# Kernel tuning notes

Hardware: AMD Instinct MI355X
Metric: run time of the kernel (lower is better)

## Reference

```python
import jax, jax.numpy as jnp
import numpy as np

SEQ, BATCH, INPUT, HIDDEN, OUTPUT = 4096, 512, 8, 30, 1


def setup_inputs() -> dict:
    key = jax.random.key(0)
    ks = jax.random.split(key, 8)
    s = 1.0 / np.sqrt(HIDDEN)  # torch LSTM/Linear init scale
    u = lambda k, shape: jax.random.uniform(k, shape, jnp.float32, -s, s)
    return {
        "x": jax.random.normal(ks[0], (SEQ, BATCH, INPUT), jnp.float32),
        "W_ih": u(ks[1], (4 * HIDDEN, INPUT)),   # gate order: i, f, g, o
        "W_hh": u(ks[2], (4 * HIDDEN, HIDDEN)),
        "b_ih": u(ks[3], (4 * HIDDEN,)),
        "b_hh": u(ks[4], (4 * HIDDEN,)),
        "W_lin": u(ks[5], (OUTPUT, HIDDEN)),
        "b_lin": u(ks[6], (OUTPUT,)),
    }


def _lstm(x, W_ih, W_hh, b_ih, b_hh):
    H = W_hh.shape[1]
    B = x.shape[1]
    # Precompute input projections for all timesteps: [S,B,4H]
    x_proj = jnp.einsum("sbi,gi->sbg", x, W_ih) + b_ih + b_hh

    def step(carry, xp_t):
        h, c = carry
        gates = xp_t + h @ W_hh.T  # [B,4H]
        i, f, g, o = jnp.split(gates, 4, axis=-1)
        i, f, o = jax.nn.sigmoid(i), jax.nn.sigmoid(f), jax.nn.sigmoid(o)
        c = f * c + i * jnp.tanh(g)
        h = o * jnp.tanh(c)
        return (h, c), h

    h0 = jnp.zeros((B, H), x.dtype)
    c0 = jnp.zeros((B, H), x.dtype)
    _, pred = jax.lax.scan(step, (h0, c0), x_proj)
    return pred  # [S,B,H]


def reference(x, W_ih, W_hh, b_ih, b_hh, W_lin, b_lin):
    pred = _lstm(x, W_ih, W_hh, b_ih, b_hh)
    # per-timestep Linear (loop in the original == one batched matmul)
    out = jnp.einsum("sbh,oh->sbo", pred, W_lin) + b_lin
    return out
```

## Files before the change

kernel.cpp:

```cpp
#include <hip/hip_runtime.h>

#define SEQ 4096
#define BATCH 512
#define INP 8
#define HID 30
#define LOG2E 1.44269504088896340736f

typedef float f32x2 __attribute__((ext_vector_type(2)));
typedef float f32x4 __attribute__((ext_vector_type(4)));
typedef unsigned uint2v __attribute__((ext_vector_type(2)));

#define RCP(v)  __builtin_amdgcn_rcpf(v)
#if __has_builtin(__builtin_amdgcn_exp2f)
#define EXP2(v) __builtin_amdgcn_exp2f(v)
#else
#define EXP2(v) exp2f(v)
#endif
#define PKFMA(a, b, c) __builtin_elementwise_fma(a, b, c)

__device__ __forceinline__ void rep_halves(float v, float& lo_rep, float& hi_rep) {
#if __has_builtin(__builtin_amdgcn_permlane32_swap)
    uint2v r = __builtin_amdgcn_permlane32_swap(
        __float_as_uint(v), __float_as_uint(v), false, false);
    lo_rep = __uint_as_float(r.x);
    hi_rep = __uint_as_float(r.y);
#else
    float other = __shfl_xor(v, 32, 64);
    bool hi = (threadIdx.x & 32) != 0;
    lo_rep = hi ? other : v;
    hi_rep = hi ? v : other;
#endif
}

template <int CTRL>
__device__ __forceinline__ float dpp_sum_step(float v) {
    return v + __uint_as_float(__builtin_amdgcn_update_dpp(
        0, (int)__float_as_uint(v), CTRL, 0xf, 0xf, true));
}

__device__ __forceinline__ float group32_reduce(float v) {
    v = dpp_sum_step<0x111>(v);
    v = dpp_sum_step<0x112>(v);
    v = dpp_sum_step<0x114>(v);
    v = dpp_sum_step<0x118>(v);
#if __has_builtin(__builtin_amdgcn_permlane16_swap)
    uint2v r = __builtin_amdgcn_permlane16_swap(
        __float_as_uint(v), __float_as_uint(v), false, false);
    return __uint_as_float(r.x) + __uint_as_float(r.y);
#else
    return v + __shfl_xor(v, 16, 64);
#endif
}

__global__ __launch_bounds__(64)
__attribute__((amdgpu_waves_per_eu(1, 1)))
void lstm_chain_kernel(
    const float* __restrict__ x,
    const float* __restrict__ W_ih,
    const float* __restrict__ W_hh,
    const float* __restrict__ b_ih,
    const float* __restrict__ b_hh,
    const float* __restrict__ W_lin,
    const float* __restrict__ b_lin,
    float* __restrict__ out)
{
    const int lane = threadIdx.x;
    const int g    = blockIdx.x;
    const int b    = (g & 7) * (BATCH / 8) + (g >> 3);
    const int j    = lane & 31;
    const int half = lane >> 5;
    const int jc   = j < HID ? j : HID - 1;
    const int ra   = half * HID + jc;
    const int rb   = 2 * HID + half * HID + jc;

    const float sA   = -LOG2E;
    const float sB   = half ? -LOG2E : 2.0f * LOG2E;
    const float sclB = half ? 1.0f : -2.0f;
    const float addB = half ? 0.0f : 1.0f;
    const float T2L  = 2.0f * LOG2E;

    f32x2 wih2_a[INP / 2], wih2_b[INP / 2];
#pragma unroll
    for (int i = 0; i < INP / 2; ++i) {
        f32x2 wa = { W_ih[ra * INP + 2 * i] * sA, W_ih[ra * INP + 2 * i + 1] * sA };
        f32x2 wb = { W_ih[rb * INP + 2 * i] * sB, W_ih[rb * INP + 2 * i + 1] * sB };
        asm volatile("" : "+v"(wa));
        asm volatile("" : "+v"(wb));
        wih2_a[i] = wa;
        wih2_b[i] = wb;
    }
    f32x2 whh2_a[HID / 2], whh2_b[HID / 2];
#pragma unroll
    for (int k = 0; k < HID / 2; ++k) {
        f32x2 wa = { W_hh[ra * HID + 2 * k] * sA, W_hh[ra * HID + 2 * k + 1] * sA };
        f32x2 wb = { W_hh[rb * HID + 2 * k] * sB, W_hh[rb * HID + 2 * k + 1] * sB };
        asm volatile("" : "+v"(wa));
        asm volatile("" : "+v"(wb));
        whh2_a[k] = wa;
        whh2_b[k] = wb;
    }
    const float bias_sa = (b_ih[ra] + b_hh[ra]) * sA;
    const float bias_sb = (b_ih[rb] + b_hh[rb]) * sB;
    const float blin    = b_lin[0];
    const float wlin    = (j < HID) ? W_lin[j] : 0.0f;

    __shared__ float s_y[SEQ];
    __shared__ __align__(16) float s_h[64];
    __shared__ __align__(16) float s_x[2 * 64 * INP];

    f32x4* sx4 = reinterpret_cast<f32x4*>(s_x);
    const f32x4* sx4c = reinterpret_cast<const f32x4*>(s_x);

    f32x2 hrf2[HID / 2];
#pragma unroll
    for (int k = 0; k < HID / 2; ++k) hrf2[k] = (f32x2){0.0f, 0.0f};
    float c = 0.0f;

    f32x4 stg0, stg1;

#define STAGELOAD(CH2) do {                                                   \
    int _b0 = (CH2) * 64 + (lane >> 1);                                       \
    int _b1 = _b0 + 32;                                                       \
    if (_b0 > SEQ - 1) _b0 = SEQ - 1;                                         \
    if (_b1 > SEQ - 1) _b1 = SEQ - 1;                                         \
    const f32x4* _p0 = (const f32x4*)(x + ((size_t)_b0 * BATCH + b) * INP) + (lane & 1); \
    const f32x4* _p1 = (const f32x4*)(x + ((size_t)_b1 * BATCH + b) * INP) + (lane & 1); \
    stg0 = *_p0;                                                              \
    stg1 = *_p1;                                                              \
} while (0)

#define STAGEWRITE(CHW) do {                                                  \
    f32x4* _d = sx4 + ((CHW) & 1) * 128;                                      \
    _d[lane]      = stg0;                                                     \
    _d[64 + lane] = stg1;                                                     \
} while (0)

#define LOADXL(XA, XB, TL) do {                                               \
    int _e = (((TL) >> 6) & 1) * 128 + ((TL) & 63) * 2;                       \
    XA = sx4c[_e];                                                            \
    XB = sx4c[_e + 1];                                                        \
} while (0)

    STAGELOAD(0);
    STAGEWRITE(0);
    STAGELOAD(1);

    f32x4 xA0, xB0, xA1, xB1, xA2, xB2, xA3, xB3;
    LOADXL(xA0, xB0, 0);  LOADXL(xA1, xB1, 1);
    LOADXL(xA2, xB2, 2);  LOADXL(xA3, xB3, 3);

    const f32x4* s_h4 = reinterpret_cast<const f32x4*>(s_h);

#define STEP(T, XA, XB) do {                                                  \
    f32x2 A0 = {bias_sa, 0.0f}, B0 = {bias_sb, 0.0f};                         \
    f32x2 A1 = {0.0f, 0.0f},    B1 = {0.0f, 0.0f};                            \
    f32x2 x01 = __builtin_shufflevector(XA, XA, 0, 1);                        \
    f32x2 x23 = __builtin_shufflevector(XA, XA, 2, 3);                        \
    f32x2 x45 = __builtin_shufflevector(XB, XB, 0, 1);                        \
    f32x2 x67 = __builtin_shufflevector(XB, XB, 2, 3);                        \
    A0 = PKFMA(x01, wih2_a[0], A0);  B0 = PKFMA(x01, wih2_b[0], B0);          \
    A1 = PKFMA(x23, wih2_a[1], A1);  B1 = PKFMA(x23, wih2_b[1], B1);          \
    A0 = PKFMA(x45, wih2_a[2], A0);  B0 = PKFMA(x45, wih2_b[2], B0);          \
    A1 = PKFMA(x67, wih2_a[3], A1);  B1 = PKFMA(x67, wih2_b[3], B1);          \
    _Pragma("unroll")                                                         \
    for (int k = 0; k < HID / 2 - 1; k += 2) {                                \
        A0 = PKFMA(hrf2[k],   whh2_a[k],   A0);                               \
        B0 = PKFMA(hrf2[k],   whh2_b[k],   B0);                               \
        A1 = PKFMA(hrf2[k+1], whh2_a[k+1], A1);                               \
        B1 = PKFMA(hrf2[k+1], whh2_b[k+1], B1);                               \
    }                                                                         \
    A0 = PKFMA(hrf2[HID/2-1], whh2_a[HID/2-1], A0);                           \
    B0 = PKFMA(hrf2[HID/2-1], whh2_b[HID/2-1], B0);                           \
    f32x2 As = A0 + A1;  float ua = As.x + As.y;                              \
    f32x2 Bs = B0 + B1;  float ub = Bs.x + Bs.y;                              \
    float Av  = RCP(1.0f + EXP2(ua));                                         \
    float sBv = RCP(1.0f + EXP2(ub));                                         \
    float Bv  = fmaf(sBv, sclB, addB);                                        \
    float ii, ff, gg, oo;                                                     \
    rep_halves(Av, ii, ff);                                                   \
    rep_halves(Bv, gg, oo);                                                   \
    c = fmaf(ff, c, ii * gg);                                                 \
    float sc = RCP(1.0f + EXP2(c * T2L));                                     \
    float h  = oo * fmaf(sc, -2.0f, 1.0f);                                    \
    s_h[lane] = h;             \
    asm volatile("" ::: "memory");         \
    float p = group32_reduce(h * wlin);                                       \
    if (lane == 31) s_y[T] = p + blin;                                        \
    f32x4 hv0 = s_h4[0], hv1 = s_h4[1], hv2 = s_h4[2], hv3 = s_h4[3];         \
    f32x4 hv4 = s_h4[4], hv5 = s_h4[5], hv6 = s_h4[6], hv7 = s_h4[7];         \
    hrf2[0]  = __builtin_shufflevector(hv0, hv0, 0, 1);                       \
    hrf2[1]  = __builtin_shufflevector(hv0, hv0, 2, 3);                       \
    hrf2[2]  = __builtin_shufflevector(hv1, hv1, 0, 1);                       \
    hrf2[3]  = __builtin_shufflevector(hv1, hv1, 2, 3);                       \
    hrf2[4]  = __builtin_shufflevector(hv2, hv2, 0, 1);                       \
    hrf2[5]  = __builtin_shufflevector(hv2, hv2, 2, 3);                       \
    hrf2[6]  = __builtin_shufflevector(hv3, hv3, 0, 1);                       \
    hrf2[7]  = __builtin_shufflevector(hv3, hv3, 2, 3);                       \
    hrf2[8]  = __builtin_shufflevector(hv4, hv4, 0, 1);                       \
    hrf2[9]  = __builtin_shufflevector(hv4, hv4, 2, 3);                       \
    hrf2[10] = __builtin_shufflevector(hv5, hv5, 0, 1);                       \
    hrf2[11] = __builtin_shufflevector(hv5, hv5, 2, 3);                       \
    hrf2[12] = __builtin_shufflevector(hv6, hv6, 0, 1);                       \
    hrf2[13] = __builtin_shufflevector(hv6, hv6, 2, 3);                       \
    hrf2[14] = __builtin_shufflevector(hv7, hv7, 0, 1);                       \
} while (0)

    for (int ch = 0; ch < SEQ / 64; ++ch) {
        STAGEWRITE(ch + 1);
        STAGELOAD(ch + 2);
        const int t0 = ch * 64;
#pragma unroll 1
        for (int tt = 0; tt < 64; tt += 4) {
            const int t = t0 + tt;
            STEP(t + 0, xA0, xB0);  LOADXL(xA0, xB0, t + 4);
            STEP(t + 1, xA1, xB1);  LOADXL(xA1, xB1, t + 5);
            STEP(t + 2, xA2, xB2);  LOADXL(xA2, xB2, t + 6);
            STEP(t + 3, xA3, xB3);  LOADXL(xA3, xB3, t + 7);
        }
    }
#undef STEP
#undef LOADXL
#undef STAGELOAD
#undef STAGEWRITE

    __syncthreads();
    const float4* s_y4 = reinterpret_cast<const float4*>(s_y);
#pragma unroll 4
    for (int it = 0; it < SEQ / 256; ++it) {
        int tbase = it * 256 + lane * 4;
        float4 v = s_y4[tbase >> 2];
        out[(size_t)(tbase + 0) * BATCH + b] = v.x;
        out[(size_t)(tbase + 1) * BATCH + b] = v.y;
        out[(size_t)(tbase + 2) * BATCH + b] = v.z;
        out[(size_t)(tbase + 3) * BATCH + b] = v.w;
    }
}

extern "C" void kernel_launch(void* const* d_in, const int* in_sizes, int n_in,
                              void* d_out, int out_size, void* d_ws, size_t ws_size,
                              hipStream_t stream) {
    const float* x     = (const float*)d_in[0];
    const float* W_ih  = (const float*)d_in[1];
    const float* W_hh  = (const float*)d_in[2];
    const float* b_ih  = (const float*)d_in[3];
    const float* b_hh  = (const float*)d_in[4];
    const float* W_lin = (const float*)d_in[5];
    const float* b_lin = (const float*)d_in[6];
    float* out = (float*)d_out;

    lstm_chain_kernel<<<dim3(BATCH), dim3(64), 0, stream>>>(
        x, W_ih, W_hh, b_ih, b_hh, W_lin, b_lin, out);
}
```

Measured before the change: 1.034 ms.

## Precompute next-step input projection off the critical path and fold tanh scaling

Moves the input-projection FMAs for step t+1 into step t, placed after the hidden-state LDS write so they overlap the LDS round trip and reduction latency. The cell state is carried pre-scaled by 2*log2e so the tanh exponent needs no multiply, and the output gate is folded into a single FMA for h. The compiler memory barrier after the s_h store is removed and the h reads are issued right after the write. This relies on LDS ordering within a single wave and adds a few registers for the precomputed accumulators.

Result: faster. 945.3 us (-8.6%).

```diff
diff --git a/kernel.cpp b/kernel.cpp
--- a/kernel.cpp
+++ b/kernel.cpp
@@ -75,9 +75,10 @@
 
     const float sA   = -LOG2E;
     const float sB   = half ? -LOG2E : 2.0f * LOG2E;
-    const float sclB = half ? 1.0f : -2.0f;
-    const float addB = half ? 0.0f : 1.0f;
     const float T2L  = 2.0f * LOG2E;
+    const float IT2L = 1.0f / (2.0f * LOG2E);
+    const float sclB2 = half ? T2L : -2.0f * T2L;
+    const float addB2 = half ? 0.0f : T2L;
 
     f32x2 wih2_a[INP / 2], wih2_b[INP / 2];
 #pragma unroll
@@ -114,7 +115,7 @@
     f32x2 hrf2[HID / 2];
 #pragma unroll
     for (int k = 0; k < HID / 2; ++k) hrf2[k] = (f32x2){0.0f, 0.0f};
-    float c = 0.0f;
+    float c2 = 0.0f;
 
     f32x4 stg0, stg1;
 
@@ -141,27 +142,34 @@
     XB = sx4c[_e + 1];                                                        \
 } while (0)
 
-    STAGELOAD(0);
-    STAGEWRITE(0);
-    STAGELOAD(1);
-
-    f32x4 xA0, xB0, xA1, xB1, xA2, xB2, xA3, xB3;
-    LOADXL(xA0, xB0, 0);  LOADXL(xA1, xB1, 1);
-    LOADXL(xA2, xB2, 2);  LOADXL(xA3, xB3, 3);
-
-    const f32x4* s_h4 = reinterpret_cast<const f32x4*>(s_h);
-
-#define STEP(T, XA, XB) do {                                                  \
-    f32x2 A0 = {bias_sa, 0.0f}, B0 = {bias_sb, 0.0f};                         \
-    f32x2 A1 = {0.0f, 0.0f},    B1 = {0.0f, 0.0f};                            \
+    f32x2 preA0, preA1, preB0, preB1;
+
+#define IHPRE(XA, XB) do {                                                    \
     f32x2 x01 = __builtin_shufflevector(XA, XA, 0, 1);                        \
     f32x2 x23 = __builtin_shufflevector(XA, XA, 2, 3);                        \
     f32x2 x45 = __builtin_shufflevector(XB, XB, 0, 1);                        \
     f32x2 x67 = __builtin_shufflevector(XB, XB, 2, 3);                        \
-    A0 = PKFMA(x01, wih2_a[0], A0);  B0 = PKFMA(x01, wih2_b[0], B0);          \
-    A1 = PKFMA(x23, wih2_a[1], A1);  B1 = PKFMA(x23, wih2_b[1], B1);          \
-    A0 = PKFMA(x45, wih2_a[2], A0);  B0 = PKFMA(x45, wih2_b[2], B0);          \
-    A1 = PKFMA(x67, wih2_a[3], A1);  B1 = PKFMA(x67, wih2_b[3], B1);          \
+    preA0 = (f32x2){bias_sa, 0.0f};  preB0 = (f32x2){bias_sb, 0.0f};          \
+    preA1 = (f32x2){0.0f, 0.0f};     preB1 = (f32x2){0.0f, 0.0f};             \
+    preA0 = PKFMA(x01, wih2_a[0], preA0);  preB0 = PKFMA(x01, wih2_b[0], preB0); \
+    preA1 = PKFMA(x23, wih2_a[1], preA1);  preB1 = PKFMA(x23, wih2_b[1], preB1); \
+    preA0 = PKFMA(x45, wih2_a[2], preA0);  preB0 = PKFMA(x45, wih2_b[2], preB0); \
+    preA1 = PKFMA(x67, wih2_a[3], preA1);  preB1 = PKFMA(x67, wih2_b[3], preB1); \
+} while (0)
+
+    STAGELOAD(0);
+    STAGEWRITE(0);
+    STAGELOAD(1);
+
+    f32x4 xA0, xB0, xA1, xB1, xA2, xB2, xA3, xB3;
+    LOADXL(xA0, xB0, 0);  LOADXL(xA1, xB1, 1);
+    LOADXL(xA2, xB2, 2);  LOADXL(xA3, xB3, 3);
+    IHPRE(xA0, xB0);
+
+    const f32x4* s_h4 = reinterpret_cast<const f32x4*>(s_h);
+
+#define STEP(T, XAn, XBn, XAl, XBl, TL) do {                                  \
+    f32x2 A0 = preA0, A1 = preA1, B0 = preB0, B1 = preB1;                     \
     _Pragma("unroll")                                                         \
     for (int k = 0; k < HID / 2 - 1; k += 2) {                                \
         A0 = PKFMA(hrf2[k],   whh2_a[k],   A0);                               \
@@ -175,19 +183,24 @@
     f32x2 Bs = B0 + B1;  float ub = Bs.x + Bs.y;                              \
     float Av  = RCP(1.0f + EXP2(ua));                                         \
     float sBv = RCP(1.0f + EXP2(ub));                                         \
-    float Bv  = fmaf(sBv, sclB, addB);                                        \
-    float ii, ff, gg, oo;                                                     \
-    rep_halves(Av, ii, ff);                                                   \
-    rep_halves(Bv, gg, oo);                                                   \
-    c = fmaf(ff, c, ii * gg);                                                 \
-    float sc = RCP(1.0f + EXP2(c * T2L));                                     \
-    float h  = oo * fmaf(sc, -2.0f, 1.0f);                                    \
-    s_h[lane] = h;             \
-    asm volatile("" ::: "memory");         \
+    float Bv2 = fmaf(sBv, sclB2, addB2);     \
+    float ii, ff, gg2, oT2;                                                   \
+    rep_halves(Av,  ii,  ff);                                                 \
+    rep_halves(Bv2, gg2, oT2);                  \
+    float oo_u = oT2 * IT2L;                                   \
+    float n2o  = oT2 * (-2.0f * IT2L);                         \
+    c2 = fmaf(ff, c2, ii * gg2);                              \
+    float sc = RCP(1.0f + EXP2(c2));                                          \
+    float h  = fmaf(sc, n2o, oo_u);                        \
+    s_h[lane] = h;                                              \
+    f32x4 hv0 = s_h4[0], hv1 = s_h4[1], hv2 = s_h4[2], hv3 = s_h4[3];         \
+    f32x4 hv4 = s_h4[4], hv5 = s_h4[5], hv6 = s_h4[6], hv7 = s_h4[7];         \
+                                 \
     float p = group32_reduce(h * wlin);                                       \
     if (lane == 31) s_y[T] = p + blin;                                        \
-    f32x4 hv0 = s_h4[0], hv1 = s_h4[1], hv2 = s_h4[2], hv3 = s_h4[3];         \
-    f32x4 hv4 = s_h4[4], hv5 = s_h4[5], hv6 = s_h4[6], hv7 = s_h4[7];         \
+    LOADXL(XAl, XBl, TL);                                                     \
+    IHPRE(XAn, XBn);                                                          \
+                                \
     hrf2[0]  = __builtin_shufflevector(hv0, hv0, 0, 1);                       \
     hrf2[1]  = __builtin_shufflevector(hv0, hv0, 2, 3);                       \
     hrf2[2]  = __builtin_shufflevector(hv1, hv1, 0, 1);                       \
@@ -212,13 +225,14 @@
 #pragma unroll 1
         for (int tt = 0; tt < 64; tt += 4) {
             const int t = t0 + tt;
-            STEP(t + 0, xA0, xB0);  LOADXL(xA0, xB0, t + 4);
-            STEP(t + 1, xA1, xB1);  LOADXL(xA1, xB1, t + 5);
-            STEP(t + 2, xA2, xB2);  LOADXL(xA2, xB2, t + 6);
-            STEP(t + 3, xA3, xB3);  LOADXL(xA3, xB3, t + 7);
+            STEP(t + 0, xA1, xB1, xA0, xB0, t + 4);
+            STEP(t + 1, xA2, xB2, xA1, xB1, t + 5);
+            STEP(t + 2, xA3, xB3, xA2, xB2, t + 6);
+            STEP(t + 3, xA0, xB0, xA3, xB3, t + 7);
         }
     }
 #undef STEP
+#undef IHPRE
 #undef LOADXL
 #undef STAGELOAD
 #undef STAGEWRITE
```

## Process two batch chains per wave with each lane computing all four gates

Applied to the files above, without the earlier changes.

Each 64-lane block now runs two independent LSTM chains, one per 32-lane half, instead of splitting one chain's gates across the halves. Each lane computes all four gates for one hidden unit, which removes the cross-half permlane exchange from the serial dependency chain. The cost is twice the packed FMAs per lane and four times as many weight registers per lane. The grid is halved to 256 blocks, so fewer waves run the serial 4096-step recurrence, at the price of longer per-step latency.

Result: slower. 1.385 ms (+34.0%).

```diff
diff --git a/kernel.cpp b/kernel.cpp
--- a/kernel.cpp
+++ b/kernel.cpp
@@ -18,18 +18,8 @@
 #endif
 #define PKFMA(a, b, c) __builtin_elementwise_fma(a, b, c)
 
-__device__ __forceinline__ void rep_halves(float v, float& lo_rep, float& hi_rep) {
-#if __has_builtin(__builtin_amdgcn_permlane32_swap)
-    uint2v r = __builtin_amdgcn_permlane32_swap(
-        __float_as_uint(v), __float_as_uint(v), false, false);
-    lo_rep = __uint_as_float(r.x);
-    hi_rep = __uint_as_float(r.y);
-#else
-    float other = __shfl_xor(v, 32, 64);
-    bool hi = (threadIdx.x & 32) != 0;
-    lo_rep = hi ? other : v;
-    hi_rep = hi ? v : other;
-#endif
+__device__ __forceinline__ f32x2 mk2(float a, float b) {
+    f32x2 r; r.x = a; r.y = b; return r;
 }
 
 template <int CTRL>
@@ -64,130 +54,151 @@
     const float* __restrict__ b_lin,
     float* __restrict__ out)
 {
-    const int lane = threadIdx.x;
-    const int g    = blockIdx.x;
-    const int b    = (g & 7) * (BATCH / 8) + (g >> 3);
-    const int j    = lane & 31;
-    const int half = lane >> 5;
-    const int jc   = j < HID ? j : HID - 1;
-    const int ra   = half * HID + jc;
-    const int rb   = 2 * HID + half * HID + jc;
-
-    const float sA   = -LOG2E;
-    const float sB   = half ? -LOG2E : 2.0f * LOG2E;
-    const float sclB = half ? 1.0f : -2.0f;
-    const float addB = half ? 0.0f : 1.0f;
-    const float T2L  = 2.0f * LOG2E;
-
-    f32x2 wih2_a[INP / 2], wih2_b[INP / 2];
-#pragma unroll
-    for (int i = 0; i < INP / 2; ++i) {
-        f32x2 wa = { W_ih[ra * INP + 2 * i] * sA, W_ih[ra * INP + 2 * i + 1] * sA };
-        f32x2 wb = { W_ih[rb * INP + 2 * i] * sB, W_ih[rb * INP + 2 * i + 1] * sB };
-        asm volatile("" : "+v"(wa));
-        asm volatile("" : "+v"(wb));
-        wih2_a[i] = wa;
-        wih2_b[i] = wb;
-    }
-    f32x2 whh2_a[HID / 2], whh2_b[HID / 2];
+    const int lane  = threadIdx.x;
+    const int g     = blockIdx.x;
+    const int b0    = 2 * ((g & 7) * 32 + (g >> 3));
+    const int chain = lane >> 5;
+    const int j     = lane & 31;
+    const int jc    = j < HID ? j : HID - 1;
+    const int ri    = jc;
+    const int rf    = HID + jc;
+    const int rg    = 2 * HID + jc;
+    const int ro    = 3 * HID + jc;
+
+    const float sS  = -LOG2E;
+    const float sG  = 2.0f * LOG2E;
+    const float T2L = 2.0f * LOG2E;
+
+    f32x2 whh_i[HID / 2], whh_f[HID / 2], whh_g[HID / 2], whh_o[HID / 2];
 #pragma unroll
     for (int k = 0; k < HID / 2; ++k) {
-        f32x2 wa = { W_hh[ra * HID + 2 * k] * sA, W_hh[ra * HID + 2 * k + 1] * sA };
-        f32x2 wb = { W_hh[rb * HID + 2 * k] * sB, W_hh[rb * HID + 2 * k + 1] * sB };
-        asm volatile("" : "+v"(wa));
-        asm volatile("" : "+v"(wb));
-        whh2_a[k] = wa;
-        whh2_b[k] = wb;
-    }
-    const float bias_sa = (b_ih[ra] + b_hh[ra]) * sA;
-    const float bias_sb = (b_ih[rb] + b_hh[rb]) * sB;
-    const float blin    = b_lin[0];
-    const float wlin    = (j < HID) ? W_lin[j] : 0.0f;
-
-    __shared__ float s_y[SEQ];
+        f32x2 wi = mk2(W_hh[ri * HID + 2 * k] * sS, W_hh[ri * HID + 2 * k + 1] * sS);
+        f32x2 wf = mk2(W_hh[rf * HID + 2 * k] * sS, W_hh[rf * HID + 2 * k + 1] * sS);
+        f32x2 wg = mk2(W_hh[rg * HID + 2 * k] * sG, W_hh[rg * HID + 2 * k + 1] * sG);
+        f32x2 wo = mk2(W_hh[ro * HID + 2 * k] * sS, W_hh[ro * HID + 2 * k + 1] * sS);
+        asm volatile("" : "+v"(wi));
+        asm volatile("" : "+v"(wf));
+        asm volatile("" : "+v"(wg));
+        asm volatile("" : "+v"(wo));
+        whh_i[k] = wi;  whh_f[k] = wf;  whh_g[k] = wg;  whh_o[k] = wo;
+    }
+    f32x2 wih_i[INP / 2], wih_f[INP / 2], wih_g[INP / 2], wih_o[INP / 2];
+#pragma unroll
+    for (int k = 0; k < INP / 2; ++k) {
+        f32x2 wi = mk2(W_ih[ri * INP + 2 * k] * sS, W_ih[ri * INP + 2 * k + 1] * sS);
+        f32x2 wf = mk2(W_ih[rf * INP + 2 * k] * sS, W_ih[rf * INP + 2 * k + 1] * sS);
+        f32x2 wg = mk2(W_ih[rg * INP + 2 * k] * sG, W_ih[rg * INP + 2 * k + 1] * sG);
+        f32x2 wo = mk2(W_ih[ro * INP + 2 * k] * sS, W_ih[ro * INP + 2 * k + 1] * sS);
+        asm volatile("" : "+v"(wi));
+        asm volatile("" : "+v"(wf));
+        asm volatile("" : "+v"(wg));
+        asm volatile("" : "+v"(wo));
+        wih_i[k] = wi;  wih_f[k] = wf;  wih_g[k] = wg;  wih_o[k] = wo;
+    }
+    const float bi = (b_ih[ri] + b_hh[ri]) * sS;
+    const float bf = (b_ih[rf] + b_hh[rf]) * sS;
+    const float bg = (b_ih[rg] + b_hh[rg]) * sG;
+    const float bo = (b_ih[ro] + b_hh[ro]) * sS;
+    const float blin = b_lin[0];
+    const float wlin = (j < HID) ? W_lin[j] : 0.0f;
+
+    __shared__ float s_y[2 * SEQ];
     __shared__ __align__(16) float s_h[64];
-    __shared__ __align__(16) float s_x[2 * 64 * INP];
+    __shared__ __align__(16) float s_x[2 * 2 * 64 * INP];
 
     f32x4* sx4 = reinterpret_cast<f32x4*>(s_x);
     const f32x4* sx4c = reinterpret_cast<const f32x4*>(s_x);
+    const f32x4* s_h4 = reinterpret_cast<const f32x4*>(s_h);
 
     f32x2 hrf2[HID / 2];
 #pragma unroll
-    for (int k = 0; k < HID / 2; ++k) hrf2[k] = (f32x2){0.0f, 0.0f};
-    float c = 0.0f;
-
-    f32x4 stg0, stg1;
+    for (int k = 0; k < HID / 2; ++k) hrf2[k] = mk2(0.0f, 0.0f);
+    float c2 = 0.0f;
+
+    f32x4 stg0, stg1, stg2, stg3;
 
 #define STAGELOAD(CH2) do {                                                   \
-    int _b0 = (CH2) * 64 + (lane >> 1);                                       \
-    int _b1 = _b0 + 32;                                                       \
-    if (_b0 > SEQ - 1) _b0 = SEQ - 1;                                         \
-    if (_b1 > SEQ - 1) _b1 = SEQ - 1;                                         \
-    const f32x4* _p0 = (const f32x4*)(x + ((size_t)_b0 * BATCH + b) * INP) + (lane & 1); \
-    const f32x4* _p1 = (const f32x4*)(x + ((size_t)_b1 * BATCH + b) * INP) + (lane & 1); \
-    stg0 = *_p0;                                                              \
-    stg1 = *_p1;                                                              \
+    int _s0 = (CH2) * 64 + (lane >> 1);                                       \
+    int _s1 = _s0 + 32;                                                       \
+    if (_s0 > SEQ - 1) _s0 = SEQ - 1;                                         \
+    if (_s1 > SEQ - 1) _s1 = SEQ - 1;                                         \
+    const f32x4* _pP0 = (const f32x4*)(x + ((size_t)_s0 * BATCH + b0) * INP) + (lane & 1);     \
+    const f32x4* _pP1 = (const f32x4*)(x + ((size_t)_s1 * BATCH + b0) * INP) + (lane & 1);     \
+    const f32x4* _pQ0 = (const f32x4*)(x + ((size_t)_s0 * BATCH + b0 + 1) * INP) + (lane & 1); \
+    const f32x4* _pQ1 = (const f32x4*)(x + ((size_t)_s1 * BATCH + b0 + 1) * INP) + (lane & 1); \
+    stg0 = *_pP0;  stg1 = *_pP1;  stg2 = *_pQ0;  stg3 = *_pQ1;                \
 } while (0)
 
 #define STAGEWRITE(CHW) do {                                                  \
-    f32x4* _d = sx4 + ((CHW) & 1) * 128;                                      \
-    _d[lane]      = stg0;                                                     \
-    _d[64 + lane] = stg1;                                                     \
-} while (0)
-
-#define LOADXL(XA, XB, TL) do {                                               \
-    int _e = (((TL) >> 6) & 1) * 128 + ((TL) & 63) * 2;                       \
-    XA = sx4c[_e];                                                            \
-    XB = sx4c[_e + 1];                                                        \
+    f32x4* _d = sx4 + ((CHW) & 1) * 256;                                      \
+    _d[lane]       = stg0;                                                    \
+    _d[64 + lane]  = stg1;                                                    \
+    _d[128 + lane] = stg2;                                                    \
+    _d[192 + lane] = stg3;                                                    \
 } while (0)
 
     STAGELOAD(0);
     STAGEWRITE(0);
     STAGELOAD(1);
 
-    f32x4 xA0, xB0, xA1, xB1, xA2, xB2, xA3, xB3;
-    LOADXL(xA0, xB0, 0);  LOADXL(xA1, xB1, 1);
-    LOADXL(xA2, xB2, 2);  LOADXL(xA3, xB3, 3);
-
-    const f32x4* s_h4 = reinterpret_cast<const f32x4*>(s_h);
-
-#define STEP(T, XA, XB) do {                                                  \
-    f32x2 A0 = {bias_sa, 0.0f}, B0 = {bias_sb, 0.0f};                         \
-    f32x2 A1 = {0.0f, 0.0f},    B1 = {0.0f, 0.0f};                            \
-    f32x2 x01 = __builtin_shufflevector(XA, XA, 0, 1);                        \
-    f32x2 x23 = __builtin_shufflevector(XA, XA, 2, 3);                        \
-    f32x2 x45 = __builtin_shufflevector(XB, XB, 0, 1);                        \
-    f32x2 x67 = __builtin_shufflevector(XB, XB, 2, 3);                        \
-    A0 = PKFMA(x01, wih2_a[0], A0);  B0 = PKFMA(x01, wih2_b[0], B0);          \
-    A1 = PKFMA(x23, wih2_a[1], A1);  B1 = PKFMA(x23, wih2_b[1], B1);          \
-    A0 = PKFMA(x45, wih2_a[2], A0);  B0 = PKFMA(x45, wih2_b[2], B0);          \
-    A1 = PKFMA(x67, wih2_a[3], A1);  B1 = PKFMA(x67, wih2_b[3], B1);          \
+#define STEP(T) do {                                                          \
+                      \
+    int _xe = (((T) >> 6) & 1) * 256 + chain * 128 + ((T) & 63) * 2;          \
+    f32x4 xa = sx4c[_xe];                                                     \
+    f32x4 xb = sx4c[_xe + 1];                                                 \
+    f32x2 ai0 = mk2(bi, 0.0f), ai1 = mk2(0.0f, 0.0f);                         \
+    f32x2 af0 = mk2(bf, 0.0f), af1 = mk2(0.0f, 0.0f);                         \
+    f32x2 ag0 = mk2(bg, 0.0f), ag1 = mk2(0.0f, 0.0f);                         \
+    f32x2 ao0 = mk2(bo, 0.0f), ao1 = mk2(0.0f, 0.0f);                         \
     _Pragma("unroll")                                                         \
     for (int k = 0; k < HID / 2 - 1; k += 2) {                                \
-        A0 = PKFMA(hrf2[k],   whh2_a[k],   A0);                               \
-        B0 = PKFMA(hrf2[k],   whh2_b[k],   B0);                               \
-        A1 = PKFMA(hrf2[k+1], whh2_a[k+1], A1);                               \
-        B1 = PKFMA(hrf2[k+1], whh2_b[k+1], B1);                               \
+        ai0 = PKFMA(hrf2[k],   whh_i[k],   ai0);                              \
+        af0 = PKFMA(hrf2[k],   whh_f[k],   af0);                              \
+        ag0 = PKFMA(hrf2[k],   whh_g[k],   ag0);                              \
+        ao0 = PKFMA(hrf2[k],   whh_o[k],   ao0);                              \
+        ai1 = PKFMA(hrf2[k+1], whh_i[k+1], ai1);                              \
+        af1 = PKFMA(hrf2[k+1], whh_f[k+1], af1);                              \
+        ag1 = PKFMA(hrf2[k+1], whh_g[k+1], ag1);                              \
+        ao1 = PKFMA(hrf2[k+1], whh_o[k+1], ao1);                              \
     }                                                                         \
-    A0 = PKFMA(hrf2[HID/2-1], whh2_a[HID/2-1], A0);                           \
-    B0 = PKFMA(hrf2[HID/2-1], whh2_b[HID/2-1], B0);                           \
-    f32x2 As = A0 + A1;  float ua = As.x + As.y;                              \
-    f32x2 Bs = B0 + B1;  float ub = Bs.x + Bs.y;                              \
-    float Av  = RCP(1.0f + EXP2(ua));                                         \
-    float sBv = RCP(1.0f + EXP2(ub));                                         \
-    float Bv  = fmaf(sBv, sclB, addB);                                        \
-    float ii, ff, gg, oo;                                                     \
-    rep_halves(Av, ii, ff);                                                   \
-    rep_halves(Bv, gg, oo);                                                   \
-    c = fmaf(ff, c, ii * gg);                                                 \
-    float sc = RCP(1.0f + EXP2(c * T2L));                                     \
-    float h  = oo * fmaf(sc, -2.0f, 1.0f);                                    \
-    s_h[lane] = h;             \
-    asm volatile("" ::: "memory");         \
+    ai0 = PKFMA(hrf2[HID/2-1], whh_i[HID/2-1], ai0);                          \
+    af0 = PKFMA(hrf2[HID/2-1], whh_f[HID/2-1], af0);                          \
+    ag0 = PKFMA(hrf2[HID/2-1], whh_g[HID/2-1], ag0);                          \
+    ao0 = PKFMA(hrf2[HID/2-1], whh_o[HID/2-1], ao0);                          \
+    f32x2 x01 = __builtin_shufflevector(xa, xa, 0, 1);                        \
+    f32x2 x23 = __builtin_shufflevector(xa, xa, 2, 3);                        \
+    f32x2 x45 = __builtin_shufflevector(xb, xb, 0, 1);                        \
+    f32x2 x67 = __builtin_shufflevector(xb, xb, 2, 3);                        \
+    ai0 = PKFMA(x01, wih_i[0], ai0);  ai1 = PKFMA(x23, wih_i[1], ai1);        \
+    af0 = PKFMA(x01, wih_f[0], af0);  af1 = PKFMA(x23, wih_f[1], af1);        \
+    ag0 = PKFMA(x01, wih_g[0], ag0);  ag1 = PKFMA(x23, wih_g[1], ag1);        \
+    ao0 = PKFMA(x01, wih_o[0], ao0);  ao1 = PKFMA(x23, wih_o[1], ao1);        \
+    ai0 = PKFMA(x45, wih_i[2], ai0);  ai1 = PKFMA(x67, wih_i[3], ai1);        \
+    af0 = PKFMA(x45, wih_f[2], af0);  af1 = PKFMA(x67, wih_f[3], af1);        \
+    ag0 = PKFMA(x45, wih_g[2], ag0);  ag1 = PKFMA(x67, wih_g[3], ag1);        \
+    ao0 = PKFMA(x45, wih_o[2], ao0);  ao1 = PKFMA(x67, wih_o[3], ao1);        \
+    f32x2 si = ai0 + ai1;  float ui = si.x + si.y;                            \
+    f32x2 sf = af0 + af1;  float uf = sf.x + sf.y;                            \
+    f32x2 sg = ag0 + ag1;  float ug = sg.x + sg.y;                            \
+    f32x2 so = ao0 + ao1;  float uo = so.x + so.y;                            \
+    float iv  = RCP(1.0f + EXP2(ui));                                         \
+    float fv  = RCP(1.0f + EXP2(uf));                                         \
+    float rgv = RCP(1.0f + EXP2(ug));                                         \
+    float ov  = RCP(1.0f + EXP2(uo));                                         \
+    float g2  = fmaf(rgv, -2.0f * T2L, T2L);                     \
+    float n2o = -2.0f * ov;                                                   \
+    c2 = fmaf(fv, c2, iv * g2);                             \
+    float sc = RCP(1.0f + EXP2(c2));                                          \
+    float h  = fmaf(sc, n2o, ov);                          \
+    s_h[lane] = h;                              \
+    f32x4 hv0 = s_h4[chain*8+0], hv1 = s_h4[chain*8+1];                       \
+    f32x4 hv2 = s_h4[chain*8+2], hv3 = s_h4[chain*8+3];                       \
+    f32x4 hv4 = s_h4[chain*8+4], hv5 = s_h4[chain*8+5];                       \
+    f32x4 hv6 = s_h4[chain*8+6], hv7 = s_h4[chain*8+7];                       \
+                                                   \
     float p = group32_reduce(h * wlin);                                       \
-    if (lane == 31) s_y[T] = p + blin;                                        \
-    f32x4 hv0 = s_h4[0], hv1 = s_h4[1], hv2 = s_h4[2], hv3 = s_h4[3];         \
-    f32x4 hv4 = s_h4[4], hv5 = s_h4[5], hv6 = s_h4[6], hv7 = s_h4[7];         \
+    if ((lane & 31) == 31) s_y[chain * SEQ + (T)] = p + blin;                 \
+                        \
     hrf2[0]  = __builtin_shufflevector(hv0, hv0, 0, 1);                       \
     hrf2[1]  = __builtin_shufflevector(hv0, hv0, 2, 3);                       \
     hrf2[2]  = __builtin_shufflevector(hv1, hv1, 0, 1);                       \
@@ -209,30 +220,28 @@
         STAGEWRITE(ch + 1);
         STAGELOAD(ch + 2);
         const int t0 = ch * 64;
-#pragma unroll 1
-        for (int tt = 0; tt < 64; tt += 4) {
-            const int t = t0 + tt;
-            STEP(t + 0, xA0, xB0);  LOADXL(xA0, xB0, t + 4);
-            STEP(t + 1, xA1, xB1);  LOADXL(xA1, xB1, t + 5);
-            STEP(t + 2, xA2, xB2);  LOADXL(xA2, xB2, t + 6);
-            STEP(t + 3, xA3, xB3);  LOADXL(xA3, xB3, t + 7);
+#pragma unroll 2
+        for (int tt = 0; tt < 64; ++tt) {
+            STEP(t0 + tt);
         }
     }
 #undef STEP
-#undef LOADXL
 #undef STAGELOAD
 #undef STAGEWRITE
 
     __syncthreads();
     const float4* s_y4 = reinterpret_cast<const float4*>(s_y);
+#pragma unroll 2
+    for (int c = 0; c < 2; ++c) {
 #pragma unroll 4
-    for (int it = 0; it < SEQ / 256; ++it) {
-        int tbase = it * 256 + lane * 4;
-        float4 v = s_y4[tbase >> 2];
-        out[(size_t)(tbase + 0) * BATCH + b] = v.x;
-        out[(size_t)(tbase + 1) * BATCH + b] = v.y;
-        out[(size_t)(tbase + 2) * BATCH + b] = v.z;
-        out[(size_t)(tbase + 3) * BATCH + b] = v.w;
+        for (int it = 0; it < SEQ / 256; ++it) {
+            int tbase = it * 256 + lane * 4;
+            float4 v = s_y4[(c * SEQ + tbase) >> 2];
+            out[(size_t)(tbase + 0) * BATCH + b0 + c] = v.x;
+            out[(size_t)(tbase + 1) * BATCH + b0 + c] = v.y;
+            out[(size_t)(tbase + 2) * BATCH + b0 + c] = v.z;
+            out[(size_t)(tbase + 3) * BATCH + b0 + c] = v.w;
+        }
     }
 }
 
@@ -248,6 +257,6 @@
     const float* b_lin = (const float*)d_in[6];
     float* out = (float*)d_out;
 
-    lstm_chain_kernel<<<dim3(BATCH), dim3(64), 0, stream>>>(
+    lstm_chain_kernel<<<dim3(BATCH / 2), dim3(64), 0, stream>>>(
         x, W_ih, W_hh, b_ih, b_hh, W_lin, b_lin, out);
 }
```
